# Kernel optimization log

Hardware: AMD Instinct MI355X
Metric: run time of the kernel (lower is better)

Reference implementation:

```python
import jax, jax.numpy as jnp
import numpy as np

B, T, D_IN, H, BR, D_OUT = 256, 500, 700, 200, 2, 35
V_TH = 1.0


def setup_inputs() -> dict:
    key = jax.random.key(0)
    ks = jax.random.split(key, 7)
    x = jax.random.normal(ks[0], (B, T, D_IN), dtype=jnp.float32)
    W_in = jax.random.normal(ks[1], (H * BR, D_IN), dtype=jnp.float32) * (1.0 / np.sqrt(D_IN))
    b_in = jax.random.normal(ks[2], (H * BR,), dtype=jnp.float32) * 0.01
    # tau_n ~ U(0, 4) per branch per neuron (as in SimpleDH_LIF init)
    tau_n = jax.random.uniform(ks[3], (H, BR), dtype=jnp.float32, minval=0.0, maxval=4.0)
    tau_m = jnp.full((H,), 2.0, dtype=jnp.float32)  # torch init: tensor(2.0) per neuron
    W_out = jax.random.normal(ks[5], (D_OUT, H), dtype=jnp.float32) * (1.0 / np.sqrt(H))
    b_out = jax.random.normal(ks[6], (D_OUT,), dtype=jnp.float32) * 0.01
    return {"x": x, "W_in": W_in, "b_in": b_in, "tau_n": tau_n,
            "tau_m": tau_m, "W_out": W_out, "b_out": b_out}


def reference(x, W_in, b_in, tau_n, tau_m, W_out, b_out):
    b, t, _ = x.shape
    # Batched input projection for all timesteps at once: (B,T,H*BR) -> (T,B,H,BR)
    branch_in = jnp.einsum('bti,oi->bto', x, W_in) + b_in
    branch_in = branch_in.reshape(b, t, H, BR).transpose(1, 0, 2, 3)

    beta = jax.nn.sigmoid(tau_n)          # (H, BR) dendritic branch decay
    alpha = jax.nn.sigmoid(tau_m)         # (H,)   soma membrane decay

    def step(carry, inp_t):
        v, i_d, counts = carry            # v:(B,H) i_d:(B,H,BR) counts:(B,H)
        i_d = beta * i_d + (1.0 - beta) * inp_t
        i_total = i_d.sum(axis=-1)        # (B,H)
        v = alpha * v + (1.0 - alpha) * i_total
        spike = (v >= V_TH).astype(v.dtype)
        v = v - spike * V_TH
        return (v, i_d, counts + spike), None

    v0 = jnp.zeros((b, H), dtype=x.dtype)
    i0 = jnp.zeros((b, H, BR), dtype=x.dtype)
    c0 = jnp.zeros((b, H), dtype=x.dtype)
    (v, i_d, spike_counts), _ = jax.lax.scan(step, (v0, i0, c0), branch_in)

    return spike_counts @ W_out.T + b_out  # (B, D_OUT)
```

## Files before the change

kernel.cpp:

```cpp
#include <hip/hip_runtime.h>

#define B_   256
#define T_   500
#define DIN  700
#define KP   704
#define H_   200
#define NO   400
#define DOUT 35
#define NKC  22

typedef _Float16 half_t;
typedef __attribute__((ext_vector_type(8))) _Float16 half8;
typedef __attribute__((ext_vector_type(4))) float floatx4;

#define SX 16.0f
#define SW 4096.0f
#define INV_S (1.0f / 65536.0f)

__device__ __forceinline__ float sigmoidf_(float x) {
    return 1.0f / (1.0f + expf(-x));
}

__global__ __launch_bounds__(256) void cvt_wfrag(
    const float* __restrict__ W, half_t* __restrict__ Whf, half_t* __restrict__ Wlf)
{
    int t = blockIdx.x * 256 + threadIdx.x;
    if (t >= NKC * 25 * 64) return;
    int lane = t & 63;
    int rest = t >> 6;
    int nfg  = rest % 25;
    int kc   = rest / 25;
    int la = lane & 15, lb = lane >> 4;
    int row = nfg * 16 + la;
    int col = kc * 32 + lb * 8;
    half8 hh, ll;
    #pragma unroll
    for (int j = 0; j < 8; ++j) {
        float v = (col + j < DIN) ? W[(size_t)row * DIN + col + j] : 0.0f;
        float s = v * SW;
        half_t h = (half_t)s;
        hh[j] = h;
        ll[j] = (half_t)(s - (float)h);
    }
    *reinterpret_cast<half8*>(&Whf[(size_t)t * 8]) = hh;
    *reinterpret_cast<half8*>(&Wlf[(size_t)t * 8]) = ll;
}

__global__ __launch_bounds__(256, 2) void dh_gemm_nolds(
    const float* __restrict__ x,
    const half_t* __restrict__ Whf, const half_t* __restrict__ Wlf,
    const float* __restrict__ bin, float* __restrict__ Y)
{
    int p = blockIdx.x;
    int xcd = p & 7, slot = p >> 3;
    int L = (xcd < 4 ? xcd * 313 : 4 * 313 + (xcd - 4) * 312) + slot;

    const int w    = threadIdx.x >> 6;
    const int lane = threadIdx.x & 63;
    const int la   = lane & 15;
    const int lb   = lane >> 4;

    const int wave = L * 4 + w;
    const int mt = wave / 5, nt = wave - mt * 5;
    const int m0 = mt * 64;
    const int o0 = nt * 80;

    floatx4 acc[4][5];
    #pragma unroll
    for (int mf = 0; mf < 4; ++mf)
        #pragma unroll
        for (int nf = 0; nf < 5; ++nf) {
            floatx4 z = {0.f, 0.f, 0.f, 0.f};
            acc[mf][nf] = z;
        }

    size_t arow[4];
    #pragma unroll
    for (int mf = 0; mf < 4; ++mf)
        arow[mf] = (size_t)(m0 + mf * 16 + la) * DIN;
    const size_t bbase = ((size_t)(nt * 5) * 64 + lane) * 8;

    float4 ra0[4][2], ra1[4][2];
    half8 b0h[5], b0l[5], b1h[5], b1l[5];
    half8 ah[4], al[4];

    auto LOADA = [&](float4 (&ra)[4][2], int kc) {
        const int col = kc * 32 + lb * 8;
        const int c2ofs = (col + 8 <= DIN) ? 4 : (692 - col);
        #pragma unroll
        for (int mf = 0; mf < 4; ++mf) {
            const float* ptr = &x[arow[mf] + col];
            ra[mf][0] = *reinterpret_cast<const float4*>(ptr);
            ra[mf][1] = *reinterpret_cast<const float4*>(ptr + c2ofs);
        }
    };
    auto LOADB = [&](half8 (&bh)[5], half8 (&bl)[5], int kc) {
        const size_t kofs = (size_t)kc * 25 * 64 * 8;
        #pragma unroll
        for (int nf = 0; nf < 5; ++nf) {
            size_t idx = bbase + kofs + (size_t)nf * 64 * 8;
            bh[nf] = *reinterpret_cast<const half8*>(&Whf[idx]);
            bl[nf] = *reinterpret_cast<const half8*>(&Wlf[idx]);
        }
    };
    auto CONV = [&](const float4 (&ra)[4][2]) {
        #pragma unroll
        for (int mf = 0; mf < 4; ++mf) {
            float vv[8];
            *reinterpret_cast<float4*>(&vv[0]) = ra[mf][0];
            *reinterpret_cast<float4*>(&vv[4]) = ra[mf][1];
            half8 hh, ll;
            #pragma unroll
            for (int j = 0; j < 8; ++j) {
                float s = vv[j] * SX;
                half_t h = (half_t)s;
                hh[j] = h;
                ll[j] = (half_t)(s - (float)h);
            }
            ah[mf] = hh;
            al[mf] = ll;
        }
    };
    auto MFMAS = [&](const half8 (&bh)[5], const half8 (&bl)[5]) {
        #pragma unroll
        for (int mf = 0; mf < 4; ++mf)
            #pragma unroll
            for (int nf = 0; nf < 5; ++nf)
                acc[mf][nf] = __builtin_amdgcn_mfma_f32_16x16x32_f16(ah[mf], bh[nf], acc[mf][nf], 0, 0, 0);
        #pragma unroll
        for (int mf = 0; mf < 4; ++mf)
            #pragma unroll
            for (int nf = 0; nf < 5; ++nf)
                acc[mf][nf] = __builtin_amdgcn_mfma_f32_16x16x32_f16(ah[mf], bl[nf], acc[mf][nf], 0, 0, 0);
        #pragma unroll
        for (int mf = 0; mf < 4; ++mf)
            #pragma unroll
            for (int nf = 0; nf < 5; ++nf)
                acc[mf][nf] = __builtin_amdgcn_mfma_f32_16x16x32_f16(al[mf], bh[nf], acc[mf][nf], 0, 0, 0);
    };

    LOADA(ra0, 0);
    LOADB(b0h, b0l, 0);
    #pragma unroll 1
    for (int kc2 = 0; kc2 < NKC; kc2 += 2) {
        LOADA(ra1, kc2 + 1);
        LOADB(b1h, b1l, kc2 + 1);
        CONV(ra0);
        MFMAS(b0h, b0l);
        if (kc2 + 2 < NKC) {
            LOADA(ra0, kc2 + 2);
            LOADB(b0h, b0l, kc2 + 2);
        }
        CONV(ra1);
        MFMAS(b1h, b1l);
    }

    float bo[5];
    #pragma unroll
    for (int nf = 0; nf < 5; ++nf) bo[nf] = bin[o0 + nf * 16 + la];

    #pragma unroll
    for (int mf = 0; mf < 4; ++mf) {
        int mbase = m0 + mf * 16 + lb * 4;
        #pragma unroll
        for (int rg = 0; rg < 4; ++rg) {
            int mm = mbase + rg;
            int bb = mm / T_;
            int tt = mm - bb * T_;
            float* yrow = &Y[((size_t)tt * B_ + bb) * NO + o0 + la];
            #pragma unroll
            for (int nf = 0; nf < 5; ++nf)
                yrow[nf * 16] = acc[mf][nf][rg] * INV_S + bo[nf];
        }
    }
}

#define BM 256
#define BN 64
#define BK 16
__global__ __launch_bounds__(256) void dh_gemm_in(
    const float* __restrict__ x, const float* __restrict__ Wt,
    const float* __restrict__ bin, float* __restrict__ Y)
{
    __shared__ float As[BK][BM + 4];
    __shared__ float Bs[BK][BN + 4];
    const int tid = threadIdx.x;
    const int tx = tid & 7;
    const int ty = tid >> 3;
    const int m0 = blockIdx.y * BM;
    const int o0 = blockIdx.x * BN;

    float acc[8][8];
    #pragma unroll
    for (int r = 0; r < 8; ++r)
        #pragma unroll
        for (int c = 0; c < 8; ++c) acc[r][c] = 0.0f;

    const int srow = tid >> 2;
    const int skq  = (tid & 3) << 2;

    for (int k0 = 0; k0 < DIN; k0 += BK) {
        float4 areg[4];
        #pragma unroll
        for (int i = 0; i < 4; ++i) {
            int idx = tid + i * 256;
            int row = idx >> 2;
            int kq  = (idx & 3) << 2;
            int kg  = k0 + kq;
            if (kg < DIN)
                areg[i] = *reinterpret_cast<const float4*>(&x[(size_t)(m0 + row) * DIN + kg]);
            else
                areg[i] = make_float4(0.f, 0.f, 0.f, 0.f);
        }
        float4 breg;
        {
            int kg = k0 + skq;
            int o  = o0 + srow;
            if (kg < DIN && o < NO)
                breg = *reinterpret_cast<const float4*>(&Wt[(size_t)o * DIN + kg]);
            else
                breg = make_float4(0.f, 0.f, 0.f, 0.f);
        }
        __syncthreads();
        #pragma unroll
        for (int i = 0; i < 4; ++i) {
            int idx = tid + i * 256;
            int row = idx >> 2;
            int kq  = (idx & 3) << 2;
            As[kq + 0][row] = areg[i].x;
            As[kq + 1][row] = areg[i].y;
            As[kq + 2][row] = areg[i].z;
            As[kq + 3][row] = areg[i].w;
        }
        Bs[skq + 0][srow] = breg.x;
        Bs[skq + 1][srow] = breg.y;
        Bs[skq + 2][srow] = breg.z;
        Bs[skq + 3][srow] = breg.w;
        __syncthreads();

        #pragma unroll
        for (int k = 0; k < BK; ++k) {
            float a[8], bb[8];
            *reinterpret_cast<float4*>(&a[0])  = *reinterpret_cast<const float4*>(&As[k][ty * 8]);
            *reinterpret_cast<float4*>(&a[4])  = *reinterpret_cast<const float4*>(&As[k][ty * 8 + 4]);
            *reinterpret_cast<float4*>(&bb[0]) = *reinterpret_cast<const float4*>(&Bs[k][tx * 8]);
            *reinterpret_cast<float4*>(&bb[4]) = *reinterpret_cast<const float4*>(&Bs[k][tx * 8 + 4]);
            #pragma unroll
            for (int r = 0; r < 8; ++r)
                #pragma unroll
                for (int c = 0; c < 8; ++c)
                    acc[r][c] = fmaf(a[r], bb[c], acc[r][c]);
        }
    }

    float bo[8];
    #pragma unroll
    for (int c = 0; c < 8; ++c) {
        int o = o0 + tx * 8 + c;
        bo[c] = (o < NO) ? bin[o] : 0.0f;
    }
    const int ob = o0 + tx * 8;
    if (ob < NO) {
        #pragma unroll
        for (int r = 0; r < 8; ++r) {
            int m = m0 + ty * 8 + r;
            int b = m / T_;
            int t = m - b * T_;
            float* yrow = &Y[((size_t)t * B_ + b) * NO];
            float4 v0 = make_float4(acc[r][0] + bo[0], acc[r][1] + bo[1],
                                    acc[r][2] + bo[2], acc[r][3] + bo[3]);
            float4 v1 = make_float4(acc[r][4] + bo[4], acc[r][5] + bo[5],
                                    acc[r][6] + bo[6], acc[r][7] + bo[7]);
            *reinterpret_cast<float4*>(&yrow[ob])     = v0;
            *reinterpret_cast<float4*>(&yrow[ob + 4]) = v1;
        }
    }
}

__global__ __launch_bounds__(64) void dh_scan(
    const float* __restrict__ Y, const float* __restrict__ tau_n,
    const float* __restrict__ tau_m, float* __restrict__ counts)
{
    int g = blockIdx.x * 64 + threadIdx.x;
    int b = g / H_;
    int h = g - b * H_;
    (void)b;
    float beta0 = sigmoidf_(tau_n[h * 2 + 0]);
    float beta1 = sigmoidf_(tau_n[h * 2 + 1]);
    float alpha = sigmoidf_(tau_m[h]);
    float omb0 = 1.0f - beta0, omb1 = 1.0f - beta1, oma = 1.0f - alpha;
    const float2* Yp = reinterpret_cast<const float2*>(Y);

    float v = 0.f, i0 = 0.f, i1 = 0.f, cnt = 0.f;
    #pragma unroll 1
    for (int t0 = 0; t0 < T_; t0 += 10) {
        float2 yb[10];
        #pragma unroll
        for (int j = 0; j < 10; ++j)
            yb[j] = Yp[(size_t)(t0 + j) * (B_ * H_) + g];
        #pragma unroll
        for (int j = 0; j < 10; ++j) {
            i0 = beta0 * i0 + omb0 * yb[j].x;
            i1 = beta1 * i1 + omb1 * yb[j].y;
            float it = i0 + i1;
            v = alpha * v + oma * it;
            if (v >= 1.0f) { v -= 1.0f; cnt += 1.0f; }
        }
    }
    counts[g] = cnt;
}

__global__ __launch_bounds__(64) void dh_out(
    const float* __restrict__ counts, const float* __restrict__ W_out,
    const float* __restrict__ b_out, float* __restrict__ out)
{
    int b = blockIdx.x;
    int o = threadIdx.x;
    if (o >= DOUT) return;
    float acc = b_out[o];
    const float* c = &counts[(size_t)b * H_];
    const float* w = &W_out[(size_t)o * H_];
    #pragma unroll 4
    for (int h = 0; h < H_; ++h)
        acc = fmaf(c[h], w[h], acc);
    out[(size_t)b * DOUT + o] = acc;
}

extern "C" void kernel_launch(void* const* d_in, const int* in_sizes, int n_in,
                              void* d_out, int out_size, void* d_ws, size_t ws_size,
                              hipStream_t stream) {
    const float* x     = (const float*)d_in[0];
    const float* W_in  = (const float*)d_in[1];
    const float* b_in  = (const float*)d_in[2];
    const float* tau_n = (const float*)d_in[3];
    const float* tau_m = (const float*)d_in[4];
    const float* W_out = (const float*)d_in[5];
    const float* b_out = (const float*)d_in[6];
    float* out = (float*)d_out;

    float* Y      = (float*)d_ws;
    float* counts = Y + (size_t)T_ * B_ * NO;

    const size_t nfrag_halves = (size_t)NKC * 25 * 64 * 8;
    size_t need = ((size_t)T_ * B_ * NO + (size_t)B_ * H_) * 4
                + 2 * nfrag_halves * 2;

    if (ws_size >= need) {
        half_t* Whf = (half_t*)(counts + (size_t)B_ * H_);
        half_t* Wlf = Whf + nfrag_halves;

        cvt_wfrag<<<(NKC * 25 * 64 + 255) / 256, 256, 0, stream>>>(W_in, Whf, Wlf);
        dh_gemm_nolds<<<2500, 256, 0, stream>>>(x, Whf, Wlf, b_in, Y);
    } else {
        dim3 g1(7, 500);
        dh_gemm_in<<<g1, 256, 0, stream>>>(x, W_in, b_in, Y);
    }

    dh_scan<<<(B_ * H_) / 64, 64, 0, stream>>>(Y, tau_n, tau_m, counts);
    dh_out<<<B_, 64, 0, stream>>>(counts, W_out, b_out, out);
}
```

Baseline: 413.1 us.

## Triple-buffer register prefetch in MFMA GEMM with explicit sched barriers

Moves the input-projection GEMM's software pipeline from double to triple register buffering. A and B fragments are now loaded three K-chunks ahead, with out-of-range loads clamped to the last chunk. The loop is made of hard sched_barrier phases that interleave conversion, loads and MFMAs, and launch bounds drop to one block per SIMD group to make room for the extra registers. The aim is to hide more global-memory latency per wave, at the cost of lower occupancy and some redundant loads at the tail.

```diff
diff --git a/kernel.cpp b/kernel.cpp
--- a/kernel.cpp
+++ b/kernel.cpp
@@ -3,7 +3,6 @@
 #define B_   256
 #define T_   500
 #define DIN  700
-#define KP   704
 #define H_   200
 #define NO   400
 #define DOUT 35
@@ -46,7 +45,7 @@
     *reinterpret_cast<half8*>(&Wlf[(size_t)t * 8]) = ll;
 }
 
-__global__ __launch_bounds__(256, 2) void dh_gemm_nolds(
+__global__ __launch_bounds__(256, 1) void dh_gemm_d3(
     const float* __restrict__ x,
     const half_t* __restrict__ Whf, const half_t* __restrict__ Wlf,
     const float* __restrict__ bin, float* __restrict__ Y)
@@ -80,11 +79,12 @@
         arow[mf] = (size_t)(m0 + mf * 16 + la) * DIN;
     const size_t bbase = ((size_t)(nt * 5) * 64 + lane) * 8;
 
-    float4 ra0[4][2], ra1[4][2];
-    half8 b0h[5], b0l[5], b1h[5], b1l[5];
+    float4 aX[4][2], aY[4][2], aZ[4][2];
+    half8 bXh[5], bXl[5], bYh[5], bYl[5], bZh[5], bZl[5];
     half8 ah[4], al[4];
 
     auto LOADA = [&](float4 (&ra)[4][2], int kc) {
+        if (kc > NKC - 1) kc = NKC - 1;
         const int col = kc * 32 + lb * 8;
         const int c2ofs = (col + 8 <= DIN) ? 4 : (692 - col);
         #pragma unroll
@@ -95,6 +95,7 @@
         }
     };
     auto LOADB = [&](half8 (&bh)[5], half8 (&bl)[5], int kc) {
+        if (kc > NKC - 1) kc = NKC - 1;
         const size_t kofs = (size_t)kc * 25 * 64 * 8;
         #pragma unroll
         for (int nf = 0; nf < 5; ++nf) {
@@ -139,21 +140,46 @@
                 acc[mf][nf] = __builtin_amdgcn_mfma_f32_16x16x32_f16(al[mf], bh[nf], acc[mf][nf], 0, 0, 0);
     };
 
-    LOADA(ra0, 0);
-    LOADB(b0h, b0l, 0);
+#define SBAR() __builtin_amdgcn_sched_barrier(0)
+
+    LOADA(aX, 0); SBAR();
+    LOADB(bXh, bXl, 0); SBAR();
+    LOADA(aY, 1); SBAR();
+    LOADB(bYh, bYl, 1); SBAR();
+    LOADA(aZ, 2); SBAR();
+    LOADB(bZh, bZl, 2); SBAR();
+
     #pragma unroll 1
-    for (int kc2 = 0; kc2 < NKC; kc2 += 2) {
-        LOADA(ra1, kc2 + 1);
-        LOADB(b1h, b1l, kc2 + 1);
-        CONV(ra0);
-        MFMAS(b0h, b0l);
-        if (kc2 + 2 < NKC) {
-            LOADA(ra0, kc2 + 2);
-            LOADB(b0h, b0l, kc2 + 2);
-        }
-        CONV(ra1);
-        MFMAS(b1h, b1l);
-    }
+    for (int I = 0; I < 7; ++I) {
+        const int kc = 3 * I;
+        SBAR();
+        CONV(aX);
+        SBAR();
+        LOADA(aX, kc + 3);
+        SBAR();
+        MFMAS(bXh, bXl);
+        SBAR();
+        LOADB(bXh, bXl, kc + 3);
+        SBAR();
+        CONV(aY);
+        SBAR();
+        LOADA(aY, kc + 4);
+        SBAR();
+        MFMAS(bYh, bYl);
+        SBAR();
+        LOADB(bYh, bYl, kc + 4);
+        SBAR();
+        CONV(aZ);
+        SBAR();
+        LOADA(aZ, kc + 5);
+        SBAR();
+        MFMAS(bZh, bZl);
+        SBAR();
+        LOADB(bZh, bZl, kc + 5);
+    }
+    SBAR();
+    CONV(aX);
+    MFMAS(bXh, bXl);
 
     float bo[5];
     #pragma unroll
@@ -173,6 +199,7 @@
                 yrow[nf * 16] = acc[mf][nf][rg] * INV_S + bo[nf];
         }
     }
+#undef SBAR
 }
 
 #define BM 256
@@ -350,7 +377,7 @@
         half_t* Wlf = Whf + nfrag_halves;
 
         cvt_wfrag<<<(NKC * 25 * 64 + 255) / 256, 256, 0, stream>>>(W_in, Whf, Wlf);
-        dh_gemm_nolds<<<2500, 256, 0, stream>>>(x, Whf, Wlf, b_in, Y);
+        dh_gemm_d3<<<2500, 256, 0, stream>>>(x, Whf, Wlf, b_in, Y);
     } else {
         dim3 g1(7, 500);
         dh_gemm_in<<<g1, 256, 0, stream>>>(x, W_in, b_in, Y);
```

New measurement: 377.7 us. 1.09x faster.

## Remap waves so a block shares the B tile and reschedule the load/MFMA pipeline

Applied to the files above, without the earlier changes.

Changes the wave-to-tile mapping so all four waves in a block share the same 80-column output slice (same W fragments) over adjacent 64-row slabs, which is meant to improve cache reuse of the weight fragments. It also drops the double-buffered B registers in favour of a single B buffer reloaded right after its MFMAs, and pins the order of loads, conversions and MFMAs with sched_barrier. MFMA phases get raised wave priority via s_setprio. Using fewer registers may help occupancy, but the single B buffer makes the MFMAs wait on B-load latency, and the clamped loads fetch redundant data on the last iterations.

```diff
diff --git a/kernel.cpp b/kernel.cpp
--- a/kernel.cpp
+++ b/kernel.cpp
@@ -3,7 +3,6 @@
 #define B_   256
 #define T_   500
 #define DIN  700
-#define KP   704
 #define H_   200
 #define NO   400
 #define DOUT 35
@@ -46,7 +45,7 @@
     *reinterpret_cast<half8*>(&Wlf[(size_t)t * 8]) = ll;
 }
 
-__global__ __launch_bounds__(256, 2) void dh_gemm_nolds(
+__global__ __launch_bounds__(256, 2) void dh_gemm_2w(
     const float* __restrict__ x,
     const half_t* __restrict__ Whf, const half_t* __restrict__ Wlf,
     const float* __restrict__ bin, float* __restrict__ Y)
@@ -54,16 +53,15 @@
     int p = blockIdx.x;
     int xcd = p & 7, slot = p >> 3;
     int L = (xcd < 4 ? xcd * 313 : 4 * 313 + (xcd - 4) * 312) + slot;
+    int by = L / 5, bx = L - by * 5;
 
     const int w    = threadIdx.x >> 6;
     const int lane = threadIdx.x & 63;
     const int la   = lane & 15;
     const int lb   = lane >> 4;
 
-    const int wave = L * 4 + w;
-    const int mt = wave / 5, nt = wave - mt * 5;
-    const int m0 = mt * 64;
-    const int o0 = nt * 80;
+    const int m0 = by * 256 + w * 64;
+    const int o0 = bx * 80;
 
     floatx4 acc[4][5];
     #pragma unroll
@@ -78,13 +76,14 @@
     #pragma unroll
     for (int mf = 0; mf < 4; ++mf)
         arow[mf] = (size_t)(m0 + mf * 16 + la) * DIN;
-    const size_t bbase = ((size_t)(nt * 5) * 64 + lane) * 8;
-
-    float4 ra0[4][2], ra1[4][2];
-    half8 b0h[5], b0l[5], b1h[5], b1l[5];
+    const size_t bbase = ((size_t)(bx * 5) * 64 + lane) * 8;
+
+    float4 aE[4][2], aO[4][2];
+    half8 bh[5], bl[5];
     half8 ah[4], al[4];
 
     auto LOADA = [&](float4 (&ra)[4][2], int kc) {
+        if (kc > NKC - 1) kc = NKC - 1;
         const int col = kc * 32 + lb * 8;
         const int c2ofs = (col + 8 <= DIN) ? 4 : (692 - col);
         #pragma unroll
@@ -94,7 +93,8 @@
             ra[mf][1] = *reinterpret_cast<const float4*>(ptr + c2ofs);
         }
     };
-    auto LOADB = [&](half8 (&bh)[5], half8 (&bl)[5], int kc) {
+    auto LOADB = [&](int kc) {
+        if (kc > NKC - 1) kc = NKC - 1;
         const size_t kofs = (size_t)kc * 25 * 64 * 8;
         #pragma unroll
         for (int nf = 0; nf < 5; ++nf) {
@@ -121,7 +121,7 @@
             al[mf] = ll;
         }
     };
-    auto MFMAS = [&](const half8 (&bh)[5], const half8 (&bl)[5]) {
+    auto MFMAS = [&]() {
         #pragma unroll
         for (int mf = 0; mf < 4; ++mf)
             #pragma unroll
@@ -139,20 +139,35 @@
                 acc[mf][nf] = __builtin_amdgcn_mfma_f32_16x16x32_f16(al[mf], bh[nf], acc[mf][nf], 0, 0, 0);
     };
 
-    LOADA(ra0, 0);
-    LOADB(b0h, b0l, 0);
+#define SBAR() __builtin_amdgcn_sched_barrier(0)
+
+    LOADA(aE, 0); SBAR();
+    LOADB(0); SBAR();
+    LOADA(aO, 1); SBAR();
+
     #pragma unroll 1
-    for (int kc2 = 0; kc2 < NKC; kc2 += 2) {
-        LOADA(ra1, kc2 + 1);
-        LOADB(b1h, b1l, kc2 + 1);
-        CONV(ra0);
-        MFMAS(b0h, b0l);
-        if (kc2 + 2 < NKC) {
-            LOADA(ra0, kc2 + 2);
-            LOADB(b0h, b0l, kc2 + 2);
-        }
-        CONV(ra1);
-        MFMAS(b1h, b1l);
+    for (int I = 0; I < 11; ++I) {
+        const int kc = 2 * I;
+        SBAR();
+        CONV(aE);
+        SBAR();
+        LOADA(aE, kc + 2);
+        SBAR();
+        __builtin_amdgcn_s_setprio(1);
+        MFMAS();
+        __builtin_amdgcn_s_setprio(0);
+        SBAR();
+        LOADB(kc + 1);
+        SBAR();
+        CONV(aO);
+        SBAR();
+        LOADA(aO, kc + 3);
+        SBAR();
+        __builtin_amdgcn_s_setprio(1);
+        MFMAS();
+        __builtin_amdgcn_s_setprio(0);
+        SBAR();
+        LOADB(kc + 2);
     }
 
     float bo[5];
@@ -173,6 +188,7 @@
                 yrow[nf * 16] = acc[mf][nf][rg] * INV_S + bo[nf];
         }
     }
+#undef SBAR
 }
 
 #define BM 256
@@ -350,7 +366,7 @@
         half_t* Wlf = Whf + nfrag_halves;
 
         cvt_wfrag<<<(NKC * 25 * 64 + 255) / 256, 256, 0, stream>>>(W_in, Whf, Wlf);
-        dh_gemm_nolds<<<2500, 256, 0, stream>>>(x, Whf, Wlf, b_in, Y);
+        dh_gemm_2w<<<2500, 256, 0, stream>>>(x, Whf, Wlf, b_in, Y);
     } else {
         dim3 g1(7, 500);
         dh_gemm_in<<<g1, 256, 0, stream>>>(x, W_in, b_in, Y);
```

New measurement: 438.7 us. 1.06x slower.
